# Performance work log

Hardware: AMD Instinct MI355X
Metric: run time of the kernel (lower is better)

Reference implementation:

```python
import jax, jax.numpy as jnp
import numpy as np

NUM_USERS = 1_000_000
NUM_ITEMS = 100_000
EMB = 128
IN_DIM = 2 * EMB
E = 8          # num_experts
H = 256        # expert_hidden
T = 2          # num_tasks
TH = 128       # tower_hidden
B = 16384


def setup_inputs() -> dict:
    key = jax.random.key(0)
    ks = jax.random.split(key, 16)
    s = lambda fan_in: 1.0 / np.sqrt(fan_in)
    return {
        "user_idx": jax.random.randint(ks[0], (B,), 0, NUM_USERS),
        "item_idx": jax.random.randint(ks[1], (B,), 0, NUM_ITEMS),
        "user_table": jax.random.normal(ks[2], (NUM_USERS, EMB), jnp.float32),
        "item_table": jax.random.normal(ks[3], (NUM_ITEMS, EMB), jnp.float32),
        "eW1": jax.random.normal(ks[4], (E, IN_DIM, H), jnp.float32) * s(IN_DIM),
        "eb1": jnp.zeros((E, H), jnp.float32),
        "eW2": jax.random.normal(ks[5], (E, H, H), jnp.float32) * s(H),
        "eb2": jnp.zeros((E, H), jnp.float32),
        "gW": jax.random.normal(ks[6], (T, IN_DIM, E), jnp.float32) * s(IN_DIM),
        "gb": jnp.zeros((T, E), jnp.float32),
        "tW1": jax.random.normal(ks[7], (T, H, TH), jnp.float32) * s(H),
        "tb1": jnp.zeros((T, TH), jnp.float32),
        "tW2": jax.random.normal(ks[8], (T, TH, 1), jnp.float32) * s(TH),
        "tb2": jnp.zeros((T, 1), jnp.float32),
    }


def reference(user_idx, item_idx, user_table, item_table,
              eW1, eb1, eW2, eb2, gW, gb, tW1, tb1, tW2, tb2):
    # Embedding lookup + concat: [B, 2*EMB]
    x = jnp.concatenate([user_table[user_idx], item_table[item_idx]], axis=1)
    # All experts batched: [B, E, H]
    h1 = jax.nn.relu(jnp.einsum('bi,eih->beh', x, eW1) + eb1[None])
    expert_out = jax.nn.relu(jnp.einsum('beh,ehk->bek', h1, eW2) + eb2[None])
    # Gates: [T, B, E] softmax over experts
    gate_w = jax.nn.softmax(jnp.einsum('bi,tie->tbe', x, gW) + gb[:, None, :], axis=-1)
    # Weighted combine: [T, B, H]
    mmoe = jnp.einsum('beh,tbe->tbh', expert_out, gate_w)
    # Towers: [T, B]
    th = jax.nn.relu(jnp.einsum('tbh,thk->tbk', mmoe, tW1) + tb1[:, None, :])
    out = (jnp.einsum('tbk,tko->tbo', th, tW2) + tb2[:, None, :]).squeeze(-1)
    return out  # [T, B] (torch returns list of T [B] tensors)
```

## Files before the change

kernel.cpp:

```cpp
#include <hip/hip_runtime.h>
#include <hip/hip_bf16.h>

typedef __bf16 bf16x8 __attribute__((ext_vector_type(8)));
typedef float f32x4 __attribute__((ext_vector_type(4)));

#define NB 16384
#define NE 8
#define NHID 256
#define NT 2

__device__ __forceinline__ unsigned short f2bf(float f) {
  unsigned u = __float_as_uint(f);
  u += 0x7fff + ((u >> 16) & 1);
  return (unsigned short)(u >> 16);
}
__device__ __forceinline__ float bf2f(unsigned short s) {
  return __uint_as_float(((unsigned)s) << 16);
}

__global__ void gather_kernel(const int* __restrict__ uidx,
                              const int* __restrict__ iidx,
                              const float* __restrict__ ut,
                              const float* __restrict__ it,
                              float* __restrict__ xf,
                              unsigned short* __restrict__ xbf) {
  int s = blockIdx.x * 4 + (threadIdx.x >> 6);
  int lane = threadIdx.x & 63;
  const float* src = (lane < 32)
      ? ut + (size_t)uidx[s] * 128 + lane * 4
      : it + (size_t)iidx[s] * 128 + (lane - 32) * 4;
  float4 v = *(const float4*)src;
  int off = s * 256 + lane * 4;
  *(float4*)(xf + off) = v;
  ushort4 bv;
  bv.x = f2bf(v.x); bv.y = f2bf(v.y); bv.z = f2bf(v.z); bv.w = f2bf(v.w);
  *(ushort4*)(xbf + off) = bv;
}

__global__ void prep_kernel(const float* __restrict__ eW1,
                            const float* __restrict__ eW2,
                            const float* __restrict__ tW1,
                            unsigned short* __restrict__ w1t,
                            unsigned short* __restrict__ w2t,
                            unsigned short* __restrict__ tw1t) {
  int blk = blockIdx.x;
  int k = threadIdx.x;
  if (blk < 2048) {
    int e = blk >> 8, n = blk & 255;
    w1t[(e * 256 + n) * 256 + k] = f2bf(eW1[(e * 256 + k) * 256 + n]);
    w2t[(e * 256 + n) * 256 + k] = f2bf(eW2[(e * 256 + k) * 256 + n]);
  } else {
    int idx = blk - 2048;
    int t = idx >> 7, n = idx & 127;
    tw1t[(t * 128 + n) * 256 + k] = f2bf(tW1[(t * 256 + k) * 128 + n]);
  }
}

__global__ void gate_kernel(const float* __restrict__ xf,
                            const float* __restrict__ gW,
                            const float* __restrict__ gb,
                            float* __restrict__ gates) {
  int idx = blockIdx.x * 256 + threadIdx.x;
  int t = idx >> 14, b = idx & 16383;
  float acc[8] = {0.f, 0.f, 0.f, 0.f, 0.f, 0.f, 0.f, 0.f};
  const float4* x4 = (const float4*)(xf + b * 256);
  const float* gwt = gW + t * 2048;
  for (int k4 = 0; k4 < 64; ++k4) {
    float4 xv = x4[k4];
    const float* gp = gwt + k4 * 32;
    float xs4[4] = {xv.x, xv.y, xv.z, xv.w};
#pragma unroll
    for (int j = 0; j < 4; ++j)
#pragma unroll
      for (int e = 0; e < 8; ++e) acc[e] += xs4[j] * gp[j * 8 + e];
  }
  float mx = -1e30f;
#pragma unroll
  for (int e = 0; e < 8; ++e) {
    acc[e] += gb[t * 8 + e];
    mx = fmaxf(mx, acc[e]);
  }
  float s = 0.f;
#pragma unroll
  for (int e = 0; e < 8; ++e) { acc[e] = expf(acc[e] - mx); s += acc[e]; }
  float inv = 1.f / s;
#pragma unroll
  for (int e = 0; e < 8; ++e) gates[idx * 8 + e] = acc[e] * inv;
}

__global__ __launch_bounds__(256, 2) void expert_kernel(
    const unsigned short* __restrict__ xbf, const unsigned short* __restrict__ w1t,
    const unsigned short* __restrict__ w2t, const float* __restrict__ eb1,
    const float* __restrict__ eb2, unsigned short* __restrict__ eo) {
  __shared__ unsigned short Xs[64 * 40];
  __shared__ unsigned short Ws[256 * 40];
  __shared__ unsigned short H1s[64 * 264];

  const int b0 = blockIdx.x * 64;
  const int e = blockIdx.y;
  const int tid = threadIdx.x;
  const int lane = tid & 63;
  const int w = tid >> 6;
  const int m = lane & 15;
  const int q = lane >> 4;
  const int k0 = q * 8;

  f32x4 zero4 = {0.f, 0.f, 0.f, 0.f};
  f32x4 acc[4][4];
#pragma unroll
  for (int rt = 0; rt < 4; ++rt)
#pragma unroll
    for (int ct = 0; ct < 4; ++ct) acc[rt][ct] = zero4;

  for (int kt = 0; kt < 8; ++kt) {
    const int kb = kt * 32;
#pragma unroll
    for (int i = 0; i < 2; ++i) {
      int idx = tid + i * 256;
      int r = idx >> 3, c = (idx & 7) * 4;
      *(ushort4*)(Xs + r * 40 + c) =
          *(const ushort4*)(xbf + (b0 + r) * 256 + kb + c);
    }
#pragma unroll
    for (int i = 0; i < 8; ++i) {
      int idx = tid + i * 256;
      int n = idx >> 3, c = (idx & 7) * 4;
      *(ushort4*)(Ws + n * 40 + c) =
          *(const ushort4*)(w1t + (e * 256 + n) * 256 + kb + c);
    }
    __syncthreads();
    bf16x8 a[4], bb[4];
#pragma unroll
    for (int rt = 0; rt < 4; ++rt)
      a[rt] = *(const bf16x8*)(Xs + (rt * 16 + m) * 40 + k0);
#pragma unroll
    for (int ct = 0; ct < 4; ++ct)
      bb[ct] = *(const bf16x8*)(Ws + (w * 64 + ct * 16 + m) * 40 + k0);
#pragma unroll
    for (int rt = 0; rt < 4; ++rt)
#pragma unroll
      for (int ct = 0; ct < 4; ++ct)
        acc[rt][ct] = __builtin_amdgcn_mfma_f32_16x16x32_bf16(
            a[rt], bb[ct], acc[rt][ct], 0, 0, 0);
    __syncthreads();
  }
#pragma unroll
  for (int ct = 0; ct < 4; ++ct) {
    int col = w * 64 + ct * 16 + m;
    float bias = eb1[e * 256 + col];
#pragma unroll
    for (int rt = 0; rt < 4; ++rt)
#pragma unroll
      for (int r = 0; r < 4; ++r) {
        int row = rt * 16 + q * 4 + r;
        H1s[row * 264 + col] = f2bf(fmaxf(acc[rt][ct][r] + bias, 0.f));
      }
  }
#pragma unroll
  for (int rt = 0; rt < 4; ++rt)
#pragma unroll
    for (int ct = 0; ct < 4; ++ct) acc[rt][ct] = zero4;
  __syncthreads();

  for (int kt = 0; kt < 8; ++kt) {
    const int kb = kt * 32;
#pragma unroll
    for (int i = 0; i < 8; ++i) {
      int idx = tid + i * 256;
      int n = idx >> 3, c = (idx & 7) * 4;
      *(ushort4*)(Ws + n * 40 + c) =
          *(const ushort4*)(w2t + (e * 256 + n) * 256 + kb + c);
    }
    __syncthreads();
    bf16x8 a[4], bb[4];
#pragma unroll
    for (int rt = 0; rt < 4; ++rt)
      a[rt] = *(const bf16x8*)(H1s + (rt * 16 + m) * 264 + kb + k0);
#pragma unroll
    for (int ct = 0; ct < 4; ++ct)
      bb[ct] = *(const bf16x8*)(Ws + (w * 64 + ct * 16 + m) * 40 + k0);
#pragma unroll
    for (int rt = 0; rt < 4; ++rt)
#pragma unroll
      for (int ct = 0; ct < 4; ++ct)
        acc[rt][ct] = __builtin_amdgcn_mfma_f32_16x16x32_bf16(
            a[rt], bb[ct], acc[rt][ct], 0, 0, 0);
    __syncthreads();
  }
#pragma unroll
  for (int ct = 0; ct < 4; ++ct) {
    int col = w * 64 + ct * 16 + m;
    float bias = eb2[e * 256 + col];
#pragma unroll
    for (int rt = 0; rt < 4; ++rt)
#pragma unroll
      for (int r = 0; r < 4; ++r) {
        int bg = b0 + rt * 16 + q * 4 + r;
        eo[(bg * 8 + e) * 256 + col] = f2bf(fmaxf(acc[rt][ct][r] + bias, 0.f));
      }
  }
}

__global__ void combine_kernel(const unsigned short* __restrict__ eo,
                               const float* __restrict__ gates,
                               unsigned short* __restrict__ mmoe) {
  int b = blockIdx.x;
  int h = threadIdx.x;
  float a0 = 0.f, a1 = 0.f;
#pragma unroll
  for (int e = 0; e < 8; ++e) {
    float v = bf2f(eo[(b * 8 + e) * 256 + h]);
    a0 += gates[b * 8 + e] * v;
    a1 += gates[(16384 + b) * 8 + e] * v;
  }
  mmoe[b * 256 + h] = f2bf(a0);
  mmoe[(16384 + b) * 256 + h] = f2bf(a1);
}

__global__ __launch_bounds__(256) void tower_kernel(
    const unsigned short* __restrict__ mmoe, const unsigned short* __restrict__ tw1t,
    const float* __restrict__ tb1, const float* __restrict__ tW2,
    const float* __restrict__ tb2, float* __restrict__ out) {
  __shared__ unsigned short MMs[32 * 264];
  __shared__ unsigned short W1s[128 * 40];
  __shared__ float red[32][2];
  const int b0 = blockIdx.x * 32;
  const int t = blockIdx.y;
  const int tid = threadIdx.x;
  const int lane = tid & 63;
  const int w = tid >> 6;
  const int m = lane & 15;
  const int q = lane >> 4;
  const int k0 = q * 8;
  const int rowbase = 16 * (w & 1);
  const int colbase = 64 * (w >> 1);

#pragma unroll
  for (int i = 0; i < 8; ++i) {
    int idx = tid + i * 256;
    int r = idx >> 6, c = (idx & 63) * 4;
    *(ushort4*)(MMs + r * 264 + c) =
        *(const ushort4*)(mmoe + (t * 16384 + b0 + r) * 256 + c);
  }
  f32x4 zero4 = {0.f, 0.f, 0.f, 0.f};
  f32x4 acc[4];
#pragma unroll
  for (int ct = 0; ct < 4; ++ct) acc[ct] = zero4;

  for (int kt = 0; kt < 8; ++kt) {
#pragma unroll
    for (int i = 0; i < 4; ++i) {
      int idx = tid + i * 256;
      int n = idx >> 3, c = (idx & 7) * 4;
      *(ushort4*)(W1s + n * 40 + c) =
          *(const ushort4*)(tw1t + (t * 128 + n) * 256 + kt * 32 + c);
    }
    __syncthreads();
    bf16x8 a = *(const bf16x8*)(MMs + (rowbase + m) * 264 + kt * 32 + k0);
#pragma unroll
    for (int ct = 0; ct < 4; ++ct) {
      bf16x8 bfr = *(const bf16x8*)(W1s + (colbase + ct * 16 + m) * 40 + k0);
      acc[ct] = __builtin_amdgcn_mfma_f32_16x16x32_bf16(a, bfr, acc[ct], 0, 0, 0);
    }
    __syncthreads();
  }
  float pr[4] = {0.f, 0.f, 0.f, 0.f};
#pragma unroll
  for (int ct = 0; ct < 4; ++ct) {
    int n = colbase + ct * 16 + m;
    float bias = tb1[t * 128 + n];
    float w2v = tW2[t * 128 + n];
#pragma unroll
    for (int r = 0; r < 4; ++r)
      pr[r] += fmaxf(acc[ct][r] + bias, 0.f) * w2v;
  }
#pragma unroll
  for (int d = 1; d < 16; d <<= 1)
#pragma unroll
    for (int r = 0; r < 4; ++r) pr[r] += __shfl_xor(pr[r], d);
  if (m == 0) {
#pragma unroll
    for (int r = 0; r < 4; ++r) red[rowbase + q * 4 + r][w >> 1] = pr[r];
  }
  __syncthreads();
  if (tid < 32) out[t * 16384 + b0 + tid] = red[tid][0] + red[tid][1] + tb2[t];
}

extern "C" void kernel_launch(void* const* d_in, const int* in_sizes, int n_in,
                              void* d_out, int out_size, void* d_ws, size_t ws_size,
                              hipStream_t stream) {
  (void)in_sizes; (void)n_in; (void)out_size; (void)ws_size;
  const int*   uidx = (const int*)d_in[0];
  const int*   iidx = (const int*)d_in[1];
  const float* ut   = (const float*)d_in[2];
  const float* it   = (const float*)d_in[3];
  const float* eW1  = (const float*)d_in[4];
  const float* eb1  = (const float*)d_in[5];
  const float* eW2  = (const float*)d_in[6];
  const float* eb2  = (const float*)d_in[7];
  const float* gW   = (const float*)d_in[8];
  const float* gb   = (const float*)d_in[9];
  const float* tW1  = (const float*)d_in[10];
  const float* tb1  = (const float*)d_in[11];
  const float* tW2  = (const float*)d_in[12];
  const float* tb2  = (const float*)d_in[13];
  float* out = (float*)d_out;

  char* p = (char*)d_ws;
  float* xf = (float*)p;             p += (size_t)NB * 256 * 4;
  unsigned short* xbf = (unsigned short*)p;  p += (size_t)NB * 256 * 2;
  unsigned short* w1t = (unsigned short*)p;  p += (size_t)NE * 256 * 256 * 2;
  unsigned short* w2t = (unsigned short*)p;  p += (size_t)NE * 256 * 256 * 2;
  unsigned short* tw1t = (unsigned short*)p; p += (size_t)NT * 128 * 256 * 2;
  float* gates = (float*)p;          p += (size_t)NT * NB * 8 * 4;
  unsigned short* eo = (unsigned short*)p;   p += (size_t)NB * NE * 256 * 2;
  unsigned short* mmoe = (unsigned short*)p; p += (size_t)NT * NB * 256 * 2;

  gather_kernel<<<NB / 4, 256, 0, stream>>>(uidx, iidx, ut, it, xf, xbf);
  prep_kernel<<<2048 + 256, 256, 0, stream>>>(eW1, eW2, tW1, w1t, w2t, tw1t);
  gate_kernel<<<(NT * NB) / 256, 256, 0, stream>>>(xf, gW, gb, gates);
  expert_kernel<<<dim3(NB / 64, NE), 256, 0, stream>>>(xbf, w1t, w2t, eb1, eb2, eo);
  combine_kernel<<<NB, 256, 0, stream>>>(eo, gates, mmoe);
  tower_kernel<<<dim3(NB / 32, NT), 256, 0, stream>>>(mmoe, tw1t, tb1, tW2, tb2, out);
}
```

Baseline: 725.3 us.

## Rework MMoE pipeline: MFMA gates, async LDS expert loads, fused combine+tower

Drops the fp32 x copy and computes gate logits with bf16 MFMA plus shuffle-based softmax. The weight transpose moves to LDS-tiled blocks and also converts gW to bf16. The expert kernel loads the whole X tile once through global_load_lds into a swizzled LDS layout and reads weights straight from global, which removes per-k-tile syncs. The combine step is fused into the tower kernel so the mmoe intermediate never round-trips through memory. Gate precision drops to bf16, and the direct global weight reads may rely on cache hits.

```diff
diff --git a/kernel.cpp b/kernel.cpp
--- a/kernel.cpp
+++ b/kernel.cpp
@@ -6,8 +6,6 @@
 
 #define NB 16384
 #define NE 8
-#define NHID 256
-#define NT 2
 
 __device__ __forceinline__ unsigned short f2bf(float f) {
   unsigned u = __float_as_uint(f);
@@ -17,12 +15,16 @@
 __device__ __forceinline__ float bf2f(unsigned short s) {
   return __uint_as_float(((unsigned)s) << 16);
 }
+__device__ __forceinline__ void async16(const void* g, void* lds) {
+  __builtin_amdgcn_global_load_lds(
+      (const __attribute__((address_space(1))) unsigned int*)g,
+      (__attribute__((address_space(3))) unsigned int*)lds, 16, 0, 0);
+}
 
 __global__ void gather_kernel(const int* __restrict__ uidx,
                               const int* __restrict__ iidx,
                               const float* __restrict__ ut,
                               const float* __restrict__ it,
-                              float* __restrict__ xf,
                               unsigned short* __restrict__ xbf) {
   int s = blockIdx.x * 4 + (threadIdx.x >> 6);
   int lane = threadIdx.x & 63;
@@ -30,260 +32,278 @@
       ? ut + (size_t)uidx[s] * 128 + lane * 4
       : it + (size_t)iidx[s] * 128 + (lane - 32) * 4;
   float4 v = *(const float4*)src;
-  int off = s * 256 + lane * 4;
-  *(float4*)(xf + off) = v;
   ushort4 bv;
   bv.x = f2bf(v.x); bv.y = f2bf(v.y); bv.z = f2bf(v.z); bv.w = f2bf(v.w);
-  *(ushort4*)(xbf + off) = bv;
-}
-
-__global__ void prep_kernel(const float* __restrict__ eW1,
-                            const float* __restrict__ eW2,
-                            const float* __restrict__ tW1,
-                            unsigned short* __restrict__ w1t,
-                            unsigned short* __restrict__ w2t,
-                            unsigned short* __restrict__ tw1t) {
+  *(ushort4*)(xbf + s * 256 + lane * 4) = bv;
+}
+
+__global__ void prep_kernel(const float* __restrict__ eW1, const float* __restrict__ eW2,
+                            const float* __restrict__ tW1, const float* __restrict__ gW,
+                            unsigned short* __restrict__ w1t, unsigned short* __restrict__ w2t,
+                            unsigned short* __restrict__ tw1t, unsigned short* __restrict__ gwt2) {
   int blk = blockIdx.x;
-  int k = threadIdx.x;
-  if (blk < 2048) {
-    int e = blk >> 8, n = blk & 255;
-    w1t[(e * 256 + n) * 256 + k] = f2bf(eW1[(e * 256 + k) * 256 + n]);
-    w2t[(e * 256 + n) * 256 + k] = f2bf(eW2[(e * 256 + k) * 256 + n]);
+  int tid = threadIdx.x;
+  if (blk == 272) {
+    int k = tid;
+#pragma unroll
+    for (int t = 0; t < 2; ++t)
+#pragma unroll
+      for (int e = 0; e < 8; ++e)
+        gwt2[(t * 8 + e) * 256 + k] = f2bf(gW[(t * 256 + k) * 8 + e]);
+    return;
+  }
+  __shared__ float T[64][68];
+  const float* src; unsigned short* dst; int src_ld;
+  if (blk < 128) {
+    int e = blk >> 4, kt = (blk >> 2) & 3, nt = blk & 3;
+    src = eW1 + ((size_t)e * 256 + kt * 64) * 256 + nt * 64;
+    dst = w1t + ((size_t)e * 256 + nt * 64) * 256 + kt * 64;
+    src_ld = 256;
+  } else if (blk < 256) {
+    int b2 = blk - 128;
+    int e = b2 >> 4, kt = (b2 >> 2) & 3, nt = b2 & 3;
+    src = eW2 + ((size_t)e * 256 + kt * 64) * 256 + nt * 64;
+    dst = w2t + ((size_t)e * 256 + nt * 64) * 256 + kt * 64;
+    src_ld = 256;
   } else {
-    int idx = blk - 2048;
-    int t = idx >> 7, n = idx & 127;
-    tw1t[(t * 128 + n) * 256 + k] = f2bf(tW1[(t * 256 + k) * 128 + n]);
-  }
-}
-
-__global__ void gate_kernel(const float* __restrict__ xf,
-                            const float* __restrict__ gW,
+    int b2 = blk - 256;
+    int t = b2 >> 3, kt = (b2 >> 1) & 3, nt = b2 & 1;
+    src = tW1 + ((size_t)t * 256 + kt * 64) * 128 + nt * 64;
+    dst = tw1t + ((size_t)t * 128 + nt * 64) * 256 + kt * 64;
+    src_ld = 128;
+  }
+  int rg = tid >> 4, cg = tid & 15;
+#pragma unroll
+  for (int i = 0; i < 4; ++i) {
+    int row = rg + i * 16, col = cg * 4;
+    float4 v = *(const float4*)(src + row * src_ld + col);
+    T[row][col] = v.x; T[row][col + 1] = v.y; T[row][col + 2] = v.z; T[row][col + 3] = v.w;
+  }
+  __syncthreads();
+#pragma unroll
+  for (int i = 0; i < 4; ++i) {
+    int n = rg + i * 16, k4 = cg * 4;
+    ushort4 o;
+    o.x = f2bf(T[k4 + 0][n]); o.y = f2bf(T[k4 + 1][n]);
+    o.z = f2bf(T[k4 + 2][n]); o.w = f2bf(T[k4 + 3][n]);
+    *(ushort4*)(dst + n * 256 + k4) = o;
+  }
+}
+
+__global__ void gate_kernel(const unsigned short* __restrict__ xbf,
+                            const unsigned short* __restrict__ gwt2,
                             const float* __restrict__ gb,
                             float* __restrict__ gates) {
-  int idx = blockIdx.x * 256 + threadIdx.x;
-  int t = idx >> 14, b = idx & 16383;
-  float acc[8] = {0.f, 0.f, 0.f, 0.f, 0.f, 0.f, 0.f, 0.f};
-  const float4* x4 = (const float4*)(xf + b * 256);
-  const float* gwt = gW + t * 2048;
-  for (int k4 = 0; k4 < 64; ++k4) {
-    float4 xv = x4[k4];
-    const float* gp = gwt + k4 * 32;
-    float xs4[4] = {xv.x, xv.y, xv.z, xv.w};
-#pragma unroll
-    for (int j = 0; j < 4; ++j)
-#pragma unroll
-      for (int e = 0; e < 8; ++e) acc[e] += xs4[j] * gp[j * 8 + e];
-  }
-  float mx = -1e30f;
-#pragma unroll
-  for (int e = 0; e < 8; ++e) {
-    acc[e] += gb[t * 8 + e];
-    mx = fmaxf(mx, acc[e]);
-  }
-  float s = 0.f;
-#pragma unroll
-  for (int e = 0; e < 8; ++e) { acc[e] = expf(acc[e] - mx); s += acc[e]; }
-  float inv = 1.f / s;
-#pragma unroll
-  for (int e = 0; e < 8; ++e) gates[idx * 8 + e] = acc[e] * inv;
+  int tid = threadIdx.x, lane = tid & 63, w = tid >> 6;
+  int m = lane & 15, q = lane >> 4;
+  int brow = blockIdx.x * 64 + w * 16;
+  const unsigned short* xp = xbf + (brow + m) * 256 + q * 8;
+  const unsigned short* gp = gwt2 + m * 256 + q * 8;
+  f32x4 acc = {0.f, 0.f, 0.f, 0.f};
+#pragma unroll
+  for (int ks = 0; ks < 8; ++ks) {
+    bf16x8 a = *(const bf16x8*)(xp + ks * 32);
+    bf16x8 b = *(const bf16x8*)(gp + ks * 32);
+    acc = __builtin_amdgcn_mfma_f32_16x16x32_bf16(a, b, acc, 0, 0, 0);
+  }
+  float bias = gb[m];
+#pragma unroll
+  for (int r = 0; r < 4; ++r) {
+    float lg = acc[r] + bias;
+    float mx = lg;
+#pragma unroll
+    for (int d = 1; d < 8; d <<= 1) mx = fmaxf(mx, __shfl_xor(mx, d));
+    float ev = __expf(lg - mx);
+    float sm = ev;
+#pragma unroll
+    for (int d = 1; d < 8; d <<= 1) sm += __shfl_xor(sm, d);
+    int b = brow + q * 4 + r;
+    gates[(((m >> 3) << 14) + b) * 8 + (m & 7)] = ev / sm;
+  }
 }
 
 __global__ __launch_bounds__(256, 2) void expert_kernel(
     const unsigned short* __restrict__ xbf, const unsigned short* __restrict__ w1t,
     const unsigned short* __restrict__ w2t, const float* __restrict__ eb1,
     const float* __restrict__ eb2, unsigned short* __restrict__ eo) {
-  __shared__ unsigned short Xs[64 * 40];
-  __shared__ unsigned short Ws[256 * 40];
-  __shared__ unsigned short H1s[64 * 264];
-
+  __shared__ unsigned short Xs[64 * 256];
+  __shared__ unsigned short H1[64 * 256];
   const int b0 = blockIdx.x * 64;
   const int e = blockIdx.y;
-  const int tid = threadIdx.x;
-  const int lane = tid & 63;
-  const int w = tid >> 6;
-  const int m = lane & 15;
-  const int q = lane >> 4;
-  const int k0 = q * 8;
-
-  f32x4 zero4 = {0.f, 0.f, 0.f, 0.f};
+  const int tid = threadIdx.x, lane = tid & 63, w = tid >> 6;
+  const int m = lane & 15, q = lane >> 4;
+
+#pragma unroll
+  for (int is = 0; is < 8; ++is) {
+    int C = is * 256 + tid;
+    int row = C >> 5, p = C & 31;
+    int l = (p & ~7) | ((p ^ row) & 7);
+    async16(xbf + (b0 + row) * 256 + l * 8,
+            (char*)Xs + (is * 256 + w * 64) * 16);
+  }
+  __syncthreads();
+
   f32x4 acc[4][4];
-#pragma unroll
-  for (int rt = 0; rt < 4; ++rt)
-#pragma unroll
-    for (int ct = 0; ct < 4; ++ct) acc[rt][ct] = zero4;
-
-  for (int kt = 0; kt < 8; ++kt) {
-    const int kb = kt * 32;
-#pragma unroll
-    for (int i = 0; i < 2; ++i) {
-      int idx = tid + i * 256;
-      int r = idx >> 3, c = (idx & 7) * 4;
-      *(ushort4*)(Xs + r * 40 + c) =
-          *(const ushort4*)(xbf + (b0 + r) * 256 + kb + c);
-    }
-#pragma unroll
-    for (int i = 0; i < 8; ++i) {
-      int idx = tid + i * 256;
-      int n = idx >> 3, c = (idx & 7) * 4;
-      *(ushort4*)(Ws + n * 40 + c) =
-          *(const ushort4*)(w1t + (e * 256 + n) * 256 + kb + c);
-    }
-    __syncthreads();
-    bf16x8 a[4], bb[4];
-#pragma unroll
-    for (int rt = 0; rt < 4; ++rt)
-      a[rt] = *(const bf16x8*)(Xs + (rt * 16 + m) * 40 + k0);
+  f32x4 z4 = {0.f, 0.f, 0.f, 0.f};
+#pragma unroll
+  for (int ct = 0; ct < 4; ++ct)
+#pragma unroll
+    for (int rt = 0; rt < 4; ++rt) acc[ct][rt] = z4;
+
+  const unsigned short* wp1 = w1t + ((size_t)(e * 256 + w * 64 + m)) * 256 + q * 8;
+#pragma unroll 2
+  for (int ks = 0; ks < 8; ++ks) {
+    bf16x8 aw[4], bx[4];
 #pragma unroll
     for (int ct = 0; ct < 4; ++ct)
-      bb[ct] = *(const bf16x8*)(Ws + (w * 64 + ct * 16 + m) * 40 + k0);
-#pragma unroll
-    for (int rt = 0; rt < 4; ++rt)
-#pragma unroll
-      for (int ct = 0; ct < 4; ++ct)
-        acc[rt][ct] = __builtin_amdgcn_mfma_f32_16x16x32_bf16(
-            a[rt], bb[ct], acc[rt][ct], 0, 0, 0);
-    __syncthreads();
+      aw[ct] = *(const bf16x8*)(wp1 + ct * 16 * 256 + ks * 32);
+#pragma unroll
+    for (int rt = 0; rt < 4; ++rt) {
+      int bl = rt * 16 + m;
+      int c = ks * 4 + q;
+      int p = (c & ~7) | ((c ^ bl) & 7);
+      bx[rt] = *(const bf16x8*)(Xs + bl * 256 + p * 8);
+    }
+#pragma unroll
+    for (int ct = 0; ct < 4; ++ct)
+#pragma unroll
+      for (int rt = 0; rt < 4; ++rt)
+        acc[ct][rt] = __builtin_amdgcn_mfma_f32_16x16x32_bf16(aw[ct], bx[rt], acc[ct][rt], 0, 0, 0);
   }
 #pragma unroll
   for (int ct = 0; ct < 4; ++ct) {
-    int col = w * 64 + ct * 16 + m;
-    float bias = eb1[e * 256 + col];
-#pragma unroll
-    for (int rt = 0; rt < 4; ++rt)
-#pragma unroll
-      for (int r = 0; r < 4; ++r) {
-        int row = rt * 16 + q * 4 + r;
-        H1s[row * 264 + col] = f2bf(fmaxf(acc[rt][ct][r] + bias, 0.f));
+    int n4 = w * 64 + ct * 16 + q * 4;
+    float4 bias = *(const float4*)(eb1 + e * 256 + n4);
+    int c = n4 >> 3;
+#pragma unroll
+    for (int rt = 0; rt < 4; ++rt) {
+      int bl = rt * 16 + m;
+      int p = (c & ~7) | ((c ^ bl) & 7);
+      ushort4 hv;
+      hv.x = f2bf(fmaxf(acc[ct][rt][0] + bias.x, 0.f));
+      hv.y = f2bf(fmaxf(acc[ct][rt][1] + bias.y, 0.f));
+      hv.z = f2bf(fmaxf(acc[ct][rt][2] + bias.z, 0.f));
+      hv.w = f2bf(fmaxf(acc[ct][rt][3] + bias.w, 0.f));
+      *(ushort4*)(H1 + bl * 256 + p * 8 + (q & 1) * 4) = hv;
+    }
+  }
+#pragma unroll
+  for (int ct = 0; ct < 4; ++ct)
+#pragma unroll
+    for (int rt = 0; rt < 4; ++rt) acc[ct][rt] = z4;
+  __syncthreads();
+
+  const unsigned short* wp2 = w2t + ((size_t)(e * 256 + w * 64 + m)) * 256 + q * 8;
+#pragma unroll 2
+  for (int ks = 0; ks < 8; ++ks) {
+    bf16x8 aw[4], bh[4];
+#pragma unroll
+    for (int ct = 0; ct < 4; ++ct)
+      aw[ct] = *(const bf16x8*)(wp2 + ct * 16 * 256 + ks * 32);
+#pragma unroll
+    for (int rt = 0; rt < 4; ++rt) {
+      int bl = rt * 16 + m;
+      int c = ks * 4 + q;
+      int p = (c & ~7) | ((c ^ bl) & 7);
+      bh[rt] = *(const bf16x8*)(H1 + bl * 256 + p * 8);
+    }
+#pragma unroll
+    for (int ct = 0; ct < 4; ++ct)
+#pragma unroll
+      for (int rt = 0; rt < 4; ++rt)
+        acc[ct][rt] = __builtin_amdgcn_mfma_f32_16x16x32_bf16(aw[ct], bh[rt], acc[ct][rt], 0, 0, 0);
+  }
+#pragma unroll
+  for (int ct = 0; ct < 4; ++ct) {
+    int n4 = w * 64 + ct * 16 + q * 4;
+    float4 bias = *(const float4*)(eb2 + e * 256 + n4);
+#pragma unroll
+    for (int rt = 0; rt < 4; ++rt) {
+      int b = b0 + rt * 16 + m;
+      ushort4 ov;
+      ov.x = f2bf(fmaxf(acc[ct][rt][0] + bias.x, 0.f));
+      ov.y = f2bf(fmaxf(acc[ct][rt][1] + bias.y, 0.f));
+      ov.z = f2bf(fmaxf(acc[ct][rt][2] + bias.z, 0.f));
+      ov.w = f2bf(fmaxf(acc[ct][rt][3] + bias.w, 0.f));
+      *(ushort4*)(eo + ((size_t)b * 8 + e) * 256 + n4) = ov;
+    }
+  }
+}
+
+__global__ __launch_bounds__(256, 2) void tower_kernel(
+    const unsigned short* __restrict__ eo, const float* __restrict__ gates,
+    const unsigned short* __restrict__ tw1t, const float* __restrict__ tb1,
+    const float* __restrict__ tW2, const float* __restrict__ tb2,
+    float* __restrict__ out) {
+  __shared__ unsigned short MM[64 * 264];
+  const int b0 = blockIdx.x * 64;
+  const int t = blockIdx.y;
+  const int tid = threadIdx.x, lane = tid & 63, w = tid >> 6;
+  const int m = lane & 15, q = lane >> 4;
+
+  {
+    int bl = tid >> 2, hq = tid & 3;
+    float g[8];
+#pragma unroll
+    for (int e = 0; e < 8; ++e) g[e] = gates[((t << 14) + b0 + bl) * 8 + e];
+    const unsigned short* ep = eo + (size_t)(b0 + bl) * 8 * 256;
+#pragma unroll
+    for (int ch = 0; ch < 4; ++ch) {
+      int h0 = hq * 64 + ch * 16;
+      float a16[16];
+#pragma unroll
+      for (int j = 0; j < 16; ++j) a16[j] = 0.f;
+#pragma unroll
+      for (int e = 0; e < 8; ++e) {
+#pragma unroll
+        for (int j = 0; j < 4; ++j) {
+          ushort4 v = *(const ushort4*)(ep + e * 256 + h0 + j * 4);
+          a16[j * 4 + 0] += g[e] * bf2f(v.x);
+          a16[j * 4 + 1] += g[e] * bf2f(v.y);
+          a16[j * 4 + 2] += g[e] * bf2f(v.z);
+          a16[j * 4 + 3] += g[e] * bf2f(v.w);
+        }
       }
-  }
-#pragma unroll
-  for (int rt = 0; rt < 4; ++rt)
-#pragma unroll
-    for (int ct = 0; ct < 4; ++ct) acc[rt][ct] = zero4;
+#pragma unroll
+      for (int j = 0; j < 4; ++j) {
+        ushort4 o;
+        o.x = f2bf(a16[j * 4 + 0]); o.y = f2bf(a16[j * 4 + 1]);
+        o.z = f2bf(a16[j * 4 + 2]); o.w = f2bf(a16[j * 4 + 3]);
+        *(ushort4*)(MM + bl * 264 + h0 + j * 4) = o;
+      }
+    }
+  }
   __syncthreads();
 
-  for (int kt = 0; kt < 8; ++kt) {
-    const int kb = kt * 32;
-#pragma unroll
-    for (int i = 0; i < 8; ++i) {
-      int idx = tid + i * 256;
-      int n = idx >> 3, c = (idx & 7) * 4;
-      *(ushort4*)(Ws + n * 40 + c) =
-          *(const ushort4*)(w2t + (e * 256 + n) * 256 + kb + c);
-    }
-    __syncthreads();
-    bf16x8 a[4], bb[4];
-#pragma unroll
-    for (int rt = 0; rt < 4; ++rt)
-      a[rt] = *(const bf16x8*)(H1s + (rt * 16 + m) * 264 + kb + k0);
-#pragma unroll
-    for (int ct = 0; ct < 4; ++ct)
-      bb[ct] = *(const bf16x8*)(Ws + (w * 64 + ct * 16 + m) * 40 + k0);
-#pragma unroll
-    for (int rt = 0; rt < 4; ++rt)
-#pragma unroll
-      for (int ct = 0; ct < 4; ++ct)
-        acc[rt][ct] = __builtin_amdgcn_mfma_f32_16x16x32_bf16(
-            a[rt], bb[ct], acc[rt][ct], 0, 0, 0);
-    __syncthreads();
-  }
-#pragma unroll
-  for (int ct = 0; ct < 4; ++ct) {
-    int col = w * 64 + ct * 16 + m;
-    float bias = eb2[e * 256 + col];
-#pragma unroll
-    for (int rt = 0; rt < 4; ++rt)
-#pragma unroll
-      for (int r = 0; r < 4; ++r) {
-        int bg = b0 + rt * 16 + q * 4 + r;
-        eo[(bg * 8 + e) * 256 + col] = f2bf(fmaxf(acc[rt][ct][r] + bias, 0.f));
-      }
-  }
-}
-
-__global__ void combine_kernel(const unsigned short* __restrict__ eo,
-                               const float* __restrict__ gates,
-                               unsigned short* __restrict__ mmoe) {
-  int b = blockIdx.x;
-  int h = threadIdx.x;
-  float a0 = 0.f, a1 = 0.f;
-#pragma unroll
-  for (int e = 0; e < 8; ++e) {
-    float v = bf2f(eo[(b * 8 + e) * 256 + h]);
-    a0 += gates[b * 8 + e] * v;
-    a1 += gates[(16384 + b) * 8 + e] * v;
-  }
-  mmoe[b * 256 + h] = f2bf(a0);
-  mmoe[(16384 + b) * 256 + h] = f2bf(a1);
-}
-
-__global__ __launch_bounds__(256) void tower_kernel(
-    const unsigned short* __restrict__ mmoe, const unsigned short* __restrict__ tw1t,
-    const float* __restrict__ tb1, const float* __restrict__ tW2,
-    const float* __restrict__ tb2, float* __restrict__ out) {
-  __shared__ unsigned short MMs[32 * 264];
-  __shared__ unsigned short W1s[128 * 40];
-  __shared__ float red[32][2];
-  const int b0 = blockIdx.x * 32;
-  const int t = blockIdx.y;
-  const int tid = threadIdx.x;
-  const int lane = tid & 63;
-  const int w = tid >> 6;
-  const int m = lane & 15;
-  const int q = lane >> 4;
-  const int k0 = q * 8;
-  const int rowbase = 16 * (w & 1);
-  const int colbase = 64 * (w >> 1);
-
-#pragma unroll
-  for (int i = 0; i < 8; ++i) {
-    int idx = tid + i * 256;
-    int r = idx >> 6, c = (idx & 63) * 4;
-    *(ushort4*)(MMs + r * 264 + c) =
-        *(const ushort4*)(mmoe + (t * 16384 + b0 + r) * 256 + c);
-  }
-  f32x4 zero4 = {0.f, 0.f, 0.f, 0.f};
-  f32x4 acc[4];
-#pragma unroll
-  for (int ct = 0; ct < 4; ++ct) acc[ct] = zero4;
-
-  for (int kt = 0; kt < 8; ++kt) {
-#pragma unroll
-    for (int i = 0; i < 4; ++i) {
-      int idx = tid + i * 256;
-      int n = idx >> 3, c = (idx & 7) * 4;
-      *(ushort4*)(W1s + n * 40 + c) =
-          *(const ushort4*)(tw1t + (t * 128 + n) * 256 + kt * 32 + c);
-    }
-    __syncthreads();
-    bf16x8 a = *(const bf16x8*)(MMs + (rowbase + m) * 264 + kt * 32 + k0);
-#pragma unroll
-    for (int ct = 0; ct < 4; ++ct) {
-      bf16x8 bfr = *(const bf16x8*)(W1s + (colbase + ct * 16 + m) * 40 + k0);
-      acc[ct] = __builtin_amdgcn_mfma_f32_16x16x32_bf16(a, bfr, acc[ct], 0, 0, 0);
-    }
-    __syncthreads();
-  }
-  float pr[4] = {0.f, 0.f, 0.f, 0.f};
-#pragma unroll
-  for (int ct = 0; ct < 4; ++ct) {
-    int n = colbase + ct * 16 + m;
-    float bias = tb1[t * 128 + n];
-    float w2v = tW2[t * 128 + n];
-#pragma unroll
-    for (int r = 0; r < 4; ++r)
-      pr[r] += fmaxf(acc[ct][r] + bias, 0.f) * w2v;
-  }
-#pragma unroll
-  for (int d = 1; d < 16; d <<= 1)
-#pragma unroll
-    for (int r = 0; r < 4; ++r) pr[r] += __shfl_xor(pr[r], d);
-  if (m == 0) {
-#pragma unroll
-    for (int r = 0; r < 4; ++r) red[rowbase + q * 4 + r][w >> 1] = pr[r];
-  }
-  __syncthreads();
-  if (tid < 32) out[t * 16384 + b0 + tid] = red[tid][0] + red[tid][1] + tb2[t];
+  const unsigned short* wp = tw1t + ((size_t)(t * 128 + m)) * 256 + q * 8;
+  const unsigned short* mp = MM + (w * 16 + m) * 264 + q * 8;
+  f32x4 acc[8];
+  f32x4 z4 = {0.f, 0.f, 0.f, 0.f};
+#pragma unroll
+  for (int ct = 0; ct < 8; ++ct) acc[ct] = z4;
+#pragma unroll 2
+  for (int ks = 0; ks < 8; ++ks) {
+    bf16x8 bm = *(const bf16x8*)(mp + ks * 32);
+#pragma unroll
+    for (int ct = 0; ct < 8; ++ct) {
+      bf16x8 aw = *(const bf16x8*)(wp + ct * 16 * 256 + ks * 32);
+      acc[ct] = __builtin_amdgcn_mfma_f32_16x16x32_bf16(aw, bm, acc[ct], 0, 0, 0);
+    }
+  }
+  float s = 0.f;
+#pragma unroll
+  for (int ct = 0; ct < 8; ++ct) {
+    int n4 = ct * 16 + q * 4;
+    float4 b1 = *(const float4*)(tb1 + t * 128 + n4);
+    float4 w2 = *(const float4*)(tW2 + t * 128 + n4);
+    s += fmaxf(acc[ct][0] + b1.x, 0.f) * w2.x;
+    s += fmaxf(acc[ct][1] + b1.y, 0.f) * w2.y;
+    s += fmaxf(acc[ct][2] + b1.z, 0.f) * w2.z;
+    s += fmaxf(acc[ct][3] + b1.w, 0.f) * w2.w;
+  }
+  s += __shfl_xor(s, 16);
+  s += __shfl_xor(s, 32);
+  if (lane < 16) out[(t << 14) + b0 + w * 16 + lane] = s + tb2[t];
 }
 
 extern "C" void kernel_launch(void* const* d_in, const int* in_sizes, int n_in,
@@ -307,19 +327,17 @@
   float* out = (float*)d_out;
 
   char* p = (char*)d_ws;
-  float* xf = (float*)p;             p += (size_t)NB * 256 * 4;
-  unsigned short* xbf = (unsigned short*)p;  p += (size_t)NB * 256 * 2;
-  unsigned short* w1t = (unsigned short*)p;  p += (size_t)NE * 256 * 256 * 2;
-  unsigned short* w2t = (unsigned short*)p;  p += (size_t)NE * 256 * 256 * 2;
-  unsigned short* tw1t = (unsigned short*)p; p += (size_t)NT * 128 * 256 * 2;
-  float* gates = (float*)p;          p += (size_t)NT * NB * 8 * 4;
-  unsigned short* eo = (unsigned short*)p;   p += (size_t)NB * NE * 256 * 2;
-  unsigned short* mmoe = (unsigned short*)p; p += (size_t)NT * NB * 256 * 2;
-
-  gather_kernel<<<NB / 4, 256, 0, stream>>>(uidx, iidx, ut, it, xf, xbf);
-  prep_kernel<<<2048 + 256, 256, 0, stream>>>(eW1, eW2, tW1, w1t, w2t, tw1t);
-  gate_kernel<<<(NT * NB) / 256, 256, 0, stream>>>(xf, gW, gb, gates);
+  unsigned short* xbf  = (unsigned short*)p; p += (size_t)NB * 256 * 2;
+  unsigned short* w1t  = (unsigned short*)p; p += (size_t)NE * 256 * 256 * 2;
+  unsigned short* w2t  = (unsigned short*)p; p += (size_t)NE * 256 * 256 * 2;
+  unsigned short* tw1t = (unsigned short*)p; p += (size_t)2 * 128 * 256 * 2;
+  unsigned short* gwt2 = (unsigned short*)p; p += (size_t)16 * 256 * 2;
+  float* gates         = (float*)p;          p += (size_t)2 * NB * 8 * 4;
+  unsigned short* eo   = (unsigned short*)p; p += (size_t)NB * NE * 256 * 2;
+
+  gather_kernel<<<NB / 4, 256, 0, stream>>>(uidx, iidx, ut, it, xbf);
+  prep_kernel<<<273, 256, 0, stream>>>(eW1, eW2, tW1, gW, w1t, w2t, tw1t, gwt2);
+  gate_kernel<<<NB / 64, 256, 0, stream>>>(xbf, gwt2, gb, gates);
   expert_kernel<<<dim3(NB / 64, NE), 256, 0, stream>>>(xbf, w1t, w2t, eb1, eb2, eo);
-  combine_kernel<<<NB, 256, 0, stream>>>(eo, gates, mmoe);
-  tower_kernel<<<dim3(NB / 32, NT), 256, 0, stream>>>(mmoe, tw1t, tb1, tW2, tb2, out);
-}
+  tower_kernel<<<dim3(NB / 64, 2), 256, 0, stream>>>(eo, gates, tw1t, tb1, tW2, tb2, out);
+}
```

Measured after the change: 777.5 us. 7.2% more time.
